# Performance work log

Hardware: AMD Instinct MI355X
Metric: run time of the kernel (lower is better)

## Reference

```python
import jax, jax.numpy as jnp
import numpy as np

B, L, D = 8, 2048, 1024
NH = 16            # n_head
HD = D // NH       # 64; attention is (HD x HD) per token in this module


def setup_inputs() -> dict:
    key = jax.random.key(0)
    ks = jax.random.split(key, 5)
    s = 0.02  # init scale for weights
    return {
        "x": jax.random.normal(ks[0], (B, L, D), jnp.float32),
        "Wq": jax.random.normal(ks[1], (D, D), jnp.float32) * s,
        "bq": jnp.zeros((D,), jnp.float32),
        "Wk": jax.random.normal(ks[2], (D, D), jnp.float32) * s,
        "bk": jnp.zeros((D,), jnp.float32),
        "Wv": jax.random.normal(ks[3], (D, D), jnp.float32) * s,
        "bv": jnp.zeros((D,), jnp.float32),
        "Wo": jax.random.normal(ks[4], (D, D), jnp.float32) * s,
        "bo": jnp.zeros((D,), jnp.float32),
    }


def reference(x, Wq, bq, Wk, bk, Wv, bv, Wo, bo):
    b, l, d = x.shape
    # QKV projections
    q = (x @ Wq + bq).reshape(b, l, HD, NH)
    k = (x @ Wk + bk).reshape(b, l, HD, NH)
    v = (x @ Wv + bv).reshape(b, l, HD, NH)
    # NOTE: module reshapes to (b, l, head_dim, n_head), so scores are
    # per-token (HD, HD) with the NH axis contracted; norm = sqrt(NH).
    norm = jnp.sqrt(jnp.asarray(NH, x.dtype))
    attn = jnp.einsum('blij,blkj->blik', q, k) / norm  # (b, l, HD, HD)
    attn = attn + 1e-06
    # mask = tril of the VALUES; jnp.where uses nonzero-as-True semantics.
    mask = jnp.tril(attn)
    attn = jnp.where(mask, attn, -jnp.inf)
    probs = jax.nn.softmax(attn, axis=-1)
    y = jnp.einsum('blik,blkj->blij', probs, v).reshape(b, l, d)
    return y @ Wo + bo
```

## Files before the change

### kernel.cpp

```cpp
#include <hip/hip_runtime.h>
#include <hip/hip_bf16.h>
#include <stdint.h>

typedef unsigned short u16;

#define Bdim 8
#define Ldim 2048
#define Ddim 1024
#define NH 16
#define HD 64
#define MTOK (Bdim*Ldim)

typedef __bf16 bf16x8 __attribute__((ext_vector_type(8)));
typedef float  f32x4  __attribute__((ext_vector_type(4)));
typedef float  f32x16 __attribute__((ext_vector_type(16)));

#define AS1 __attribute__((address_space(1)))
#define AS3 __attribute__((address_space(3)))

__device__ __forceinline__ void gload_lds16(const void* g, void* l) {
  __builtin_amdgcn_global_load_lds((const AS1 void*)g, (AS3 void*)l, 16, 0, 0);
}

__device__ __forceinline__ u16 f2bf(float f) {
  uint32_t u = __builtin_bit_cast(uint32_t, f);
  u += 0x7fffu + ((u >> 16) & 1u);
  return (u16)(u >> 16);
}
__device__ __forceinline__ uint32_t pkpair(float lo, float hi) {
  return (uint32_t)f2bf(lo) | ((uint32_t)f2bf(hi) << 16);
}

__global__ __launch_bounds__(256) void conv_f32_bf16(const float* __restrict__ in,
                                                     u16* __restrict__ out, int n4) {
  int i = blockIdx.x * 256 + threadIdx.x;
  if (i < n4) {
    float4 v = ((const float4*)in)[i];
    uint32_t w0 = (uint32_t)f2bf(v.x) | ((uint32_t)f2bf(v.y) << 16);
    uint32_t w1 = (uint32_t)f2bf(v.z) | ((uint32_t)f2bf(v.w) << 16);
    ((uint2*)out)[i] = make_uint2(w0, w1);
  }
}

__global__ __launch_bounds__(256) void conv_transpose_w(const float* __restrict__ W,
                                                        u16* __restrict__ Wt) {
  __shared__ float t[32][33];
  int tx = threadIdx.x & 31, ty = threadIdx.x >> 5;
  int k0 = blockIdx.x * 32, n0 = blockIdx.y * 32;
  #pragma unroll
  for (int i = 0; i < 32; i += 8)
    t[ty + i][tx] = W[(size_t)(k0 + ty + i) * Ddim + n0 + tx];
  __syncthreads();
  #pragma unroll
  for (int i = 0; i < 32; i += 8)
    Wt[(size_t)(n0 + ty + i) * Ddim + k0 + tx] = f2bf(t[tx][ty + i]);
}

template <int FUSED>
__global__ __launch_bounds__(512, 4) void gemmDP(const u16* __restrict__ A,
                                                 const u16* __restrict__ Bt,
                                                 const float* __restrict__ b0p,
                                                 const float* __restrict__ b1p,
                                                 const float* __restrict__ b2p,
                                                 void* __restrict__ o0,
                                                 void* __restrict__ o1,
                                                 void* __restrict__ o2) {
  __shared__ alignas(16) u16 LP[24576];
  const int tid = threadIdx.x;
  const int wid = tid >> 6, lane = tid & 63;
  const int wr = wid >> 2, wc = wid & 3;
  const int fr = lane & 15, fh = lane >> 4;
  const int key = (fr >> 1) & 3;

  const int bid = blockIdx.x;
  const int xcd = bid & 7, idx = bid >> 3;
  const int mt = xcd * 16 + (idx & 15);
  const int nt = idx >> 4;
  const int m0 = mt * 128, n0g = nt * 256;

  const int sr  = tid >> 2;
  const int sgc = ((tid & 3) ^ ((tid >> 3) & 3)) * 8;
  const u16* aS  = A  + (size_t)(m0 + sr)        * 1024 + sgc;
  const u16* bS0 = Bt + (size_t)(n0g + sr)       * 1024 + sgc;
  const u16* bS1 = Bt + (size_t)(n0g + 128 + sr) * 1024 + sgc;
  const int ldA = wid * 512;

#define STG(T, B_) do {                                                        \
    gload_lds16(aS  + (T) * 32, LP + (B_) * 12288 + ldA);                      \
    gload_lds16(bS0 + (T) * 32, LP + (B_) * 12288 + 4096 + ldA);               \
    gload_lds16(bS1 + (T) * 32, LP + (B_) * 12288 + 8192 + ldA);               \
  } while (0)

#define WAITV(N) asm volatile("s_waitcnt vmcnt(" #N ")" ::: "memory")
#define BAR() __builtin_amdgcn_s_barrier()

  f32x4 acc[4][4] = {};

#define COMPUTE(B_) do {                                                       \
    const u16* la_ = LP + (B_) * 12288;                                        \
    const u16* lb_ = la_ + 4096;                                               \
    const int p_ = (fh ^ key) * 8;                                             \
    bf16x8 bf_[4];                                                             \
    _Pragma("unroll")                                                          \
    for (int n_ = 0; n_ < 4; ++n_)                                             \
      bf_[n_] = *(const bf16x8*)(lb_ + (wc * 64 + n_ * 16 + fr) * 32 + p_);    \
    __builtin_amdgcn_s_setprio(1);                                             \
    _Pragma("unroll")                                                          \
    for (int m_ = 0; m_ < 4; ++m_) {                                           \
      bf16x8 am_ = *(const bf16x8*)(la_ + (wr * 64 + m_ * 16 + fr) * 32 + p_); \
      _Pragma("unroll")                                                        \
      for (int n_ = 0; n_ < 4; ++n_)                                           \
        acc[m_][n_] = __builtin_amdgcn_mfma_f32_16x16x32_bf16(                 \
            am_, bf_[n_], acc[m_][n_], 0, 0, 0);                               \
    }                                                                          \
    __builtin_amdgcn_s_setprio(0);                                             \
  } while (0)

  STG(0, 0);
  #pragma unroll 1
  for (int t = 0; t < 31; ++t) {
    const int b = t & 1;
    BAR();
    STG(t + 1, b ^ 1);
    WAITV(3);
    BAR();
    COMPUTE(b);
  }
  BAR();
  WAITV(0);
  BAR();
  COMPUTE(1);
  __syncthreads();

  if (FUSED) {
    const int which = nt >> 2;
    const int n0l = (nt & 3) * 256;
    const float* bias = which == 0 ? b0p : which == 1 ? b1p : b2p;
    u16* Out = (u16*)(which == 0 ? o0 : which == 1 ? o1 : o2);
    u16* Ct = LP;
    #pragma unroll 1
    for (int h = 0; h < 2; ++h) {
      if (h) __syncthreads();
      if ((wc >> 1) == h) {
        #pragma unroll
        for (int n = 0; n < 4; ++n) {
          float bvv = bias[n0l + h * 128 + (wc & 1) * 64 + n * 16 + fr];
          #pragma unroll
          for (int m = 0; m < 4; ++m)
            #pragma unroll
            for (int r = 0; r < 4; ++r)
              Ct[(wr * 64 + m * 16 + fh * 4 + r) * 136 +
                 (wc & 1) * 64 + n * 16 + fr] = f2bf(acc[m][n][r] + bvv);
        }
      }
      __syncthreads();
      if (which != 2) {
        #pragma unroll
        for (int j = 0; j < 4; ++j) {
          int unit = j * 512 + tid, row = unit >> 4, c8 = unit & 15;
          uint4 v = *(const uint4*)(Ct + row * 136 + c8 * 8);
          *(uint4*)(Out + (size_t)(m0 + row) * Ddim + n0l + h * 128 + c8 * 8) = v;
        }
      } else {
        #pragma unroll
        for (int j = 0; j < 4; ++j) {
          int unit = j * 512 + tid, row = unit >> 4, i = unit & 15;
          u16 tmp[8];
          #pragma unroll
          for (int jj = 0; jj < 8; ++jj) tmp[jj] = Ct[row * 136 + i + 16 * jj];
          *(uint4*)(Out + (size_t)(m0 + row) * Ddim + i * 64 +
                    (n0l >> 4) + h * 8) = *(uint4*)tmp;
        }
      }
      __syncthreads();
    }
  } else {
    float* Cf = (float*)LP;
    float* Out = (float*)o0;
    #pragma unroll 1
    for (int h = 0; h < 4; ++h) {
      if (h) __syncthreads();
      if (wc == h) {
        #pragma unroll
        for (int n = 0; n < 4; ++n) {
          float bvv = b0p[n0g + h * 64 + n * 16 + fr];
          #pragma unroll
          for (int m = 0; m < 4; ++m)
            #pragma unroll
            for (int r = 0; r < 4; ++r)
              Cf[(wr * 64 + m * 16 + fh * 4 + r) * 68 + n * 16 + fr] =
                  acc[m][n][r] + bvv;
        }
      }
      __syncthreads();
      #pragma unroll
      for (int j = 0; j < 4; ++j) {
        int unit = j * 512 + tid, row = unit >> 4, c4 = unit & 15;
        float4 v = *(const float4*)(Cf + row * 68 + c4 * 4);
        *(float4*)(Out + (size_t)(m0 + row) * Ddim + n0g + h * 64 + c4 * 4) = v;
      }
      __syncthreads();
    }
  }
#undef STG
#undef WAITV
#undef BAR
#undef COMPUTE
}

__global__ __launch_bounds__(256) void attn_mfma(const u16* __restrict__ Q,
                                                 const u16* __restrict__ Kb,
                                                 const u16* __restrict__ Vt,
                                                 u16* __restrict__ Y) {
  const int wid = threadIdx.x >> 6, lane = threadIdx.x & 63;
  const int tok = blockIdx.x * 4 + wid;
  const size_t base = (size_t)tok * Ddim;
  const int hi = lane >> 5, c31 = lane & 31;

  const bf16x8 kf0 = *(const bf16x8*)(Kb + base + (size_t)c31 * NH + hi * 8);
  const bf16x8 kf1 = *(const bf16x8*)(Kb + base + (size_t)(32 + c31) * NH + hi * 8);
  const bf16x8 qf0 = *(const bf16x8*)(Q  + base + (size_t)c31 * NH + hi * 8);
  const bf16x8 qf1 = *(const bf16x8*)(Q  + base + (size_t)(32 + c31) * NH + hi * 8);
  bf16x8 bv[4];
  #pragma unroll
  for (int c = 0; c < 4; ++c)
    bv[c] = *(const bf16x8*)(Vt + base + (size_t)(lane & 15) * HD + c * 16 + hi * 8);

  const f32x16 z = {};
  f32x16 s00 = __builtin_amdgcn_mfma_f32_32x32x16_bf16(kf0, qf0, z, 0, 0, 0);
  f32x16 s01 = __builtin_amdgcn_mfma_f32_32x32x16_bf16(kf0, qf1, z, 0, 0, 0);
  f32x16 s11 = __builtin_amdgcn_mfma_f32_32x32x16_bf16(kf1, qf1, z, 0, 0, 0);

  float a[16], b0[16], b1[16];
  float mA = -3e38f, mB = -3e38f;
  #pragma unroll
  for (int r = 0; r < 16; ++r) {
    const int kl = (r & 3) + 8 * (r >> 2) + 4 * hi;
    const bool keep = kl <= c31;
    float v00 = fmaf(s00[r], 0.25f, 1e-6f);
    float v01 = fmaf(s01[r], 0.25f, 1e-6f);
    float v11 = fmaf(s11[r], 0.25f, 1e-6f);
    a[r]  = keep ? v00 : -3e38f;
    b0[r] = v01;
    b1[r] = keep ? v11 : -3e38f;
    mA = fmaxf(mA, a[r]);
    mB = fmaxf(mB, fmaxf(b0[r], b1[r]));
  }
  mA = fmaxf(mA, __shfl_xor(mA, 32, 64));
  mB = fmaxf(mB, __shfl_xor(mB, 32, 64));
  float sA = 0.f, sB = 0.f;
  #pragma unroll
  for (int r = 0; r < 16; ++r) {
    a[r]  = __expf(a[r]  - mA);  sA += a[r];
    b0[r] = __expf(b0[r] - mB);
    b1[r] = __expf(b1[r] - mB);  sB += b0[r] + b1[r];
  }
  sA += __shfl_xor(sA, 32, 64);
  sB += __shfl_xor(sB, 32, 64);
  const float iA = __builtin_amdgcn_rcpf(sA);
  const float iB = __builtin_amdgcn_rcpf(sB);

  uint32_t pA[4][2], pB0[4][2], pB1[4][2];
  #pragma unroll
  for (int m = 0; m < 4; ++m)
    #pragma unroll
    for (int t = 0; t < 2; ++t) {
      pA [m][t] = pkpair(a [4*m+2*t] * iA, a [4*m+2*t+1] * iA);
      pB0[m][t] = pkpair(b0[4*m+2*t] * iB, b0[4*m+2*t+1] * iB);
      pB1[m][t] = pkpair(b1[4*m+2*t] * iB, b1[4*m+2*t+1] * iB);
    }

#define AFRAG(dst, src, cp) do {                                              \
    uint32_t k0_ = hi ? src[2*(cp)+1][0] : src[2*(cp)][0];                    \
    uint32_t k1_ = hi ? src[2*(cp)+1][1] : src[2*(cp)][1];                    \
    uint32_t s0_ = hi ? src[2*(cp)][0]   : src[2*(cp)+1][0];                  \
    uint32_t s1_ = hi ? src[2*(cp)][1]   : src[2*(cp)+1][1];                  \
    uint32_t r0_ = (uint32_t)__shfl_xor((int)s0_, 32, 64);                    \
    uint32_t r1_ = (uint32_t)__shfl_xor((int)s1_, 32, 64);                    \
    union { uint32_t w[4]; bf16x8 v; } u_;                                    \
    u_.w[0] = hi ? r0_ : k0_;  u_.w[1] = hi ? r1_ : k1_;                      \
    u_.w[2] = hi ? k0_ : r0_;  u_.w[3] = hi ? k1_ : r1_;                      \
    dst = u_.v;                                                               \
  } while (0)

  f32x16 y0 = {}, y1 = {};
  bf16x8 af;
  AFRAG(af, pA, 0);  y0 = __builtin_amdgcn_mfma_f32_32x32x16_bf16(af, bv[0], y0, 0, 0, 0);
  AFRAG(af, pA, 1);  y0 = __builtin_amdgcn_mfma_f32_32x32x16_bf16(af, bv[1], y0, 0, 0, 0);
  AFRAG(af, pB0, 0); y1 = __builtin_amdgcn_mfma_f32_32x32x16_bf16(af, bv[0], y1, 0, 0, 0);
  AFRAG(af, pB0, 1); y1 = __builtin_amdgcn_mfma_f32_32x32x16_bf16(af, bv[1], y1, 0, 0, 0);
  AFRAG(af, pB1, 0); y1 = __builtin_amdgcn_mfma_f32_32x32x16_bf16(af, bv[2], y1, 0, 0, 0);
  AFRAG(af, pB1, 1); y1 = __builtin_amdgcn_mfma_f32_32x32x16_bf16(af, bv[3], y1, 0, 0, 0);
#undef AFRAG

  if (c31 < 16) {
    #pragma unroll
    for (int r = 0; r < 16; ++r) {
      const int row = (r & 3) + 8 * (r >> 2) + 4 * hi;
      Y[base + (size_t)row * NH + c31]        = f2bf(y0[r]);
      Y[base + (size_t)(32 + row) * NH + c31] = f2bf(y1[r]);
    }
  }
}

extern "C" void kernel_launch(void* const* d_in, const int* in_sizes, int n_in,
                              void* d_out, int out_size, void* d_ws, size_t ws_size,
                              hipStream_t stream) {
  const float* x  = (const float*)d_in[0];
  const float* Wq = (const float*)d_in[1];
  const float* bq = (const float*)d_in[2];
  const float* Wk = (const float*)d_in[3];
  const float* bk = (const float*)d_in[4];
  const float* Wv = (const float*)d_in[5];
  const float* bv = (const float*)d_in[6];
  const float* Wo = (const float*)d_in[7];
  const float* bo = (const float*)d_in[8];
  float* out = (float*)d_out;

  u16* xb = (u16*)d_ws;
  u16* Wt = xb + (size_t)MTOK * Ddim;
  u16* Qb = Wt + 4ull * Ddim * Ddim;
  u16* Kb = Qb + (size_t)MTOK * Ddim;
  u16* Vb = Kb + (size_t)MTOK * Ddim;
  u16* Yb = xb;

  conv_f32_bf16<<<(MTOK * Ddim / 4 + 255) / 256, 256, 0, stream>>>(x, xb, MTOK * Ddim / 4);

  dim3 tg(Ddim / 32, Ddim / 32);
  conv_transpose_w<<<tg, 256, 0, stream>>>(Wq, Wt + 0ull * Ddim * Ddim);
  conv_transpose_w<<<tg, 256, 0, stream>>>(Wk, Wt + 1ull * Ddim * Ddim);
  conv_transpose_w<<<tg, 256, 0, stream>>>(Wv, Wt + 2ull * Ddim * Ddim);
  conv_transpose_w<<<tg, 256, 0, stream>>>(Wo, Wt + 3ull * Ddim * Ddim);

  gemmDP<1><<<dim3(1536), 512, 0, stream>>>(xb, Wt, bq, bk, bv, Qb, Kb, Vb);

  attn_mfma<<<MTOK / 4, 256, 0, stream>>>(Qb, Kb, Vb, Yb);

  gemmDP<0><<<dim3(512), 512, 0, stream>>>(Yb, Wt + 3ull * Ddim * Ddim,
                                           bo, bo, bo, out, out, out);
}
```

Before: 219.3 us.

## Restructure GEMM to 4-wave blocks with triple-buffered LDS and wider per-wave tiles

```diff
diff --git a/kernel.cpp b/kernel.cpp
--- a/kernel.cpp
+++ b/kernel.cpp
@@ -57,79 +57,84 @@
 }
 
 template <int FUSED>
-__global__ __launch_bounds__(512, 4) void gemmDP(const u16* __restrict__ A,
-                                                 const u16* __restrict__ Bt,
-                                                 const float* __restrict__ b0p,
-                                                 const float* __restrict__ b1p,
-                                                 const float* __restrict__ b2p,
-                                                 void* __restrict__ o0,
-                                                 void* __restrict__ o1,
-                                                 void* __restrict__ o2) {
-  __shared__ alignas(16) u16 LP[24576];
+__global__ __launch_bounds__(256, 2) void gemmT(const u16* __restrict__ A,
+                                                const u16* __restrict__ Bt,
+                                                const float* __restrict__ b0p,
+                                                const float* __restrict__ b1p,
+                                                const float* __restrict__ b2p,
+                                                void* __restrict__ o0,
+                                                void* __restrict__ o1,
+                                                void* __restrict__ o2) {
+  __shared__ alignas(16) u16 LP[36864];
   const int tid = threadIdx.x;
   const int wid = tid >> 6, lane = tid & 63;
-  const int wr = wid >> 2, wc = wid & 3;
+  const int wc = wid;
   const int fr = lane & 15, fh = lane >> 4;
-  const int key = (fr >> 1) & 3;
+  constexpr int NTN = FUSED ? 12 : 4;
 
   const int bid = blockIdx.x;
   const int xcd = bid & 7, idx = bid >> 3;
-  const int mt = xcd * 16 + (idx & 15);
-  const int nt = idx >> 4;
-  const int m0 = mt * 128, n0g = nt * 256;
-
-  const int sr  = tid >> 2;
-  const int sgc = ((tid & 3) ^ ((tid >> 3) & 3)) * 8;
-  const u16* aS  = A  + (size_t)(m0 + sr)        * 1024 + sgc;
-  const u16* bS0 = Bt + (size_t)(n0g + sr)       * 1024 + sgc;
-  const u16* bS1 = Bt + (size_t)(n0g + 128 + sr) * 1024 + sgc;
-  const int ldA = wid * 512;
+  const int mt8 = idx & 7, rest = idx >> 3;
+  const int nt = rest % NTN, chunk = rest / NTN;
+  const int m0 = (xcd * 16 + chunk * 8 + mt8) * 128;
+  const int n0g = nt * 256;
+
+  const int cks = (fh ^ ((fr >> 1) & 3)) * 8;
+  const int srow = tid >> 2;
+  const int sblk = (tid & 3) ^ ((srow >> 1) & 3);
+  const u16* aS = A  + (size_t)(m0  + srow) * 1024 + sblk * 8;
+  const u16* bS = Bt + (size_t)(n0g + srow) * 1024 + sblk * 8;
 
 #define STG(T, B_) do {                                                        \
-    gload_lds16(aS  + (T) * 32, LP + (B_) * 12288 + ldA);                      \
-    gload_lds16(bS0 + (T) * 32, LP + (B_) * 12288 + 4096 + ldA);               \
-    gload_lds16(bS1 + (T) * 32, LP + (B_) * 12288 + 8192 + ldA);               \
+    u16* d_ = (u16*)LP + (B_) * 12288 + (wid << 9);                            \
+    const u16* a_ = aS + (size_t)(T) * 32;                                     \
+    const u16* b_ = bS + (size_t)(T) * 32;                                     \
+    gload_lds16(a_,          d_);                                              \
+    gload_lds16(a_ + 65536,  d_ + 2048);                                       \
+    gload_lds16(b_,          d_ + 4096);                                       \
+    gload_lds16(b_ + 65536,  d_ + 6144);                                       \
+    gload_lds16(b_ + 131072, d_ + 8192);                                       \
+    gload_lds16(b_ + 196608, d_ + 10240);                                      \
   } while (0)
-
-#define WAITV(N) asm volatile("s_waitcnt vmcnt(" #N ")" ::: "memory")
-#define BAR() __builtin_amdgcn_s_barrier()
-
-  f32x4 acc[4][4] = {};
+#define BAR() do { asm volatile("" ::: "memory");                              \
+                   __builtin_amdgcn_s_barrier();                               \
+                   asm volatile("" ::: "memory"); } while (0)
+
+  f32x4 acc[8][4] = {};
 
 #define COMPUTE(B_) do {                                                       \
     const u16* la_ = LP + (B_) * 12288;                                        \
     const u16* lb_ = la_ + 4096;                                               \
-    const int p_ = (fh ^ key) * 8;                                             \
-    bf16x8 bf_[4];                                                             \
+    bf16x8 bf_[4], af_[8];                                                     \
     _Pragma("unroll")                                                          \
     for (int n_ = 0; n_ < 4; ++n_)                                             \
-      bf_[n_] = *(const bf16x8*)(lb_ + (wc * 64 + n_ * 16 + fr) * 32 + p_);    \
+      bf_[n_] = *(const bf16x8*)(lb_ + (wc * 64 + n_ * 16 + fr) * 32 + cks);   \
+    _Pragma("unroll")                                                          \
+    for (int m_ = 0; m_ < 8; ++m_)                                             \
+      af_[m_] = *(const bf16x8*)(la_ + (m_ * 16 + fr) * 32 + cks);             \
     __builtin_amdgcn_s_setprio(1);                                             \
     _Pragma("unroll")                                                          \
-    for (int m_ = 0; m_ < 4; ++m_) {                                           \
-      bf16x8 am_ = *(const bf16x8*)(la_ + (wr * 64 + m_ * 16 + fr) * 32 + p_); \
+    for (int m_ = 0; m_ < 8; ++m_)                                             \
       _Pragma("unroll")                                                        \
       for (int n_ = 0; n_ < 4; ++n_)                                           \
         acc[m_][n_] = __builtin_amdgcn_mfma_f32_16x16x32_bf16(                 \
-            am_, bf_[n_], acc[m_][n_], 0, 0, 0);                               \
-    }                                                                          \
+            af_[m_], bf_[n_], acc[m_][n_], 0, 0, 0);                           \
     __builtin_amdgcn_s_setprio(0);                                             \
   } while (0)
 
   STG(0, 0);
+  STG(1, 1);
   #pragma unroll 1
-  for (int t = 0; t < 31; ++t) {
-    const int b = t & 1;
+  for (int t = 0; t < 32; ++t) {
+    const int b = t % 3;
     BAR();
-    STG(t + 1, b ^ 1);
-    WAITV(3);
+    if (t < 30) STG(t + 2, (t + 2) % 3);
+    if (t < 30)       { asm volatile("s_waitcnt vmcnt(12)" ::: "memory"); }
+    else if (t == 30) { asm volatile("s_waitcnt vmcnt(6)"  ::: "memory"); }
+    else              { asm volatile("s_waitcnt vmcnt(0)"  ::: "memory"); }
     BAR();
     COMPUTE(b);
   }
-  BAR();
-  WAITV(0);
-  BAR();
-  COMPUTE(1);
   __syncthreads();
 
   if (FUSED) {
@@ -141,69 +146,64 @@
     #pragma unroll 1
     for (int h = 0; h < 2; ++h) {
       if (h) __syncthreads();
-      if ((wc >> 1) == h) {
+      #pragma unroll
+      for (int n = 0; n < 4; ++n) {
+        float bvv = bias[n0l + wc * 64 + n * 16 + fr];
         #pragma unroll
-        for (int n = 0; n < 4; ++n) {
-          float bvv = bias[n0l + h * 128 + (wc & 1) * 64 + n * 16 + fr];
+        for (int m = 0; m < 4; ++m)
           #pragma unroll
-          for (int m = 0; m < 4; ++m)
-            #pragma unroll
-            for (int r = 0; r < 4; ++r)
-              Ct[(wr * 64 + m * 16 + fh * 4 + r) * 136 +
-                 (wc & 1) * 64 + n * 16 + fr] = f2bf(acc[m][n][r] + bvv);
-        }
+          for (int r = 0; r < 4; ++r)
+            Ct[(m * 16 + fh * 4 + r) * 264 + wc * 64 + n * 16 + fr] =
+                f2bf(acc[h * 4 + m][n][r] + bvv);
       }
       __syncthreads();
       if (which != 2) {
         #pragma unroll
-        for (int j = 0; j < 4; ++j) {
-          int unit = j * 512 + tid, row = unit >> 4, c8 = unit & 15;
-          uint4 v = *(const uint4*)(Ct + row * 136 + c8 * 8);
-          *(uint4*)(Out + (size_t)(m0 + row) * Ddim + n0l + h * 128 + c8 * 8) = v;
+        for (int j = 0; j < 8; ++j) {
+          int u = j * 256 + tid, lr = u >> 5, c8 = u & 31;
+          uint4 v = *(const uint4*)(Ct + lr * 264 + c8 * 8);
+          *(uint4*)(Out + (size_t)(m0 + h * 64 + lr) * Ddim + n0l + c8 * 8) = v;
         }
       } else {
         #pragma unroll
         for (int j = 0; j < 4; ++j) {
-          int unit = j * 512 + tid, row = unit >> 4, i = unit & 15;
-          u16 tmp[8];
+          int u = j * 256 + tid, lr = u >> 4, ii = u & 15;
+          u16 tmp[16];
           #pragma unroll
-          for (int jj = 0; jj < 8; ++jj) tmp[jj] = Ct[row * 136 + i + 16 * jj];
-          *(uint4*)(Out + (size_t)(m0 + row) * Ddim + i * 64 +
-                    (n0l >> 4) + h * 8) = *(uint4*)tmp;
+          for (int jj = 0; jj < 16; ++jj)
+            tmp[jj] = Ct[lr * 264 + ii + 16 * jj];
+          u16* dst = Out + (size_t)(m0 + h * 64 + lr) * Ddim + ii * 64 + (n0l >> 4);
+          *(uint4*)dst = *(uint4*)tmp;
+          *(uint4*)(dst + 8) = *(uint4*)(tmp + 8);
         }
       }
-      __syncthreads();
     }
   } else {
     float* Cf = (float*)LP;
     float* Out = (float*)o0;
     #pragma unroll 1
-    for (int h = 0; h < 4; ++h) {
+    for (int h = 0; h < 2; ++h) {
       if (h) __syncthreads();
-      if (wc == h) {
+      #pragma unroll
+      for (int n = 0; n < 4; ++n) {
+        float bvv = b0p[n0g + wc * 64 + n * 16 + fr];
         #pragma unroll
-        for (int n = 0; n < 4; ++n) {
-          float bvv = b0p[n0g + h * 64 + n * 16 + fr];
+        for (int m = 0; m < 4; ++m)
           #pragma unroll
-          for (int m = 0; m < 4; ++m)
-            #pragma unroll
-            for (int r = 0; r < 4; ++r)
-              Cf[(wr * 64 + m * 16 + fh * 4 + r) * 68 + n * 16 + fr] =
-                  acc[m][n][r] + bvv;
-        }
+          for (int r = 0; r < 4; ++r)
+            Cf[(m * 16 + fh * 4 + r) * 264 + wc * 64 + n * 16 + fr] =
+                acc[h * 4 + m][n][r] + bvv;
       }
       __syncthreads();
       #pragma unroll
-      for (int j = 0; j < 4; ++j) {
-        int unit = j * 512 + tid, row = unit >> 4, c4 = unit & 15;
-        float4 v = *(const float4*)(Cf + row * 68 + c4 * 4);
-        *(float4*)(Out + (size_t)(m0 + row) * Ddim + n0g + h * 64 + c4 * 4) = v;
+      for (int j = 0; j < 16; ++j) {
+        int u = j * 256 + tid, lr = u >> 6, c4 = u & 63;
+        float4 v = *(const float4*)(Cf + lr * 264 + c4 * 4);
+        *(float4*)(Out + (size_t)(m0 + h * 64 + lr) * Ddim + n0g + c4 * 4) = v;
       }
-      __syncthreads();
     }
   }
 #undef STG
-#undef WAITV
 #undef BAR
 #undef COMPUTE
 }
@@ -332,10 +332,10 @@
   conv_transpose_w<<<tg, 256, 0, stream>>>(Wv, Wt + 2ull * Ddim * Ddim);
   conv_transpose_w<<<tg, 256, 0, stream>>>(Wo, Wt + 3ull * Ddim * Ddim);
 
-  gemmDP<1><<<dim3(1536), 512, 0, stream>>>(xb, Wt, bq, bk, bv, Qb, Kb, Vb);
+  gemmT<1><<<dim3(1536), 256, 0, stream>>>(xb, Wt, bq, bk, bv, Qb, Kb, Vb);
 
   attn_mfma<<<MTOK / 4, 256, 0, stream>>>(Qb, Kb, Vb, Yb);
 
-  gemmDP<0><<<dim3(512), 512, 0, stream>>>(Yb, Wt + 3ull * Ddim * Ddim,
-                                           bo, bo, bo, out, out, out);
-}
+  gemmT<0><<<dim3(512), 256, 0, stream>>>(Yb, Wt + 3ull * Ddim * Ddim,
+                                          bo, bo, bo, out, out, out);
+}
```

Result: slower. 315.1 us (+43.7%).
